# Kernel optimization log

Measured on AMD Instinct MI355X. Metric: run time of the kernel, lower is better.

## Reference

```python
import jax, jax.numpy as jnp
import numpy as np

N_NODES = 100000
N_EDGES = 3200000
IN_FEAT = 256   # dim * decoder_heads = 128 * 2
HEADS = 2
N_CLASSES = 8
CURV = 1.0
NEG_SLOPE = 0.2
EPS = 1e-15


def setup_inputs() -> dict:
    key = jax.random.key(0)
    ks = jax.random.split(key, 7)
    x = jax.random.normal(ks[0], (N_NODES, IN_FEAT), dtype=jnp.float32) * 0.1
    edge_index = jax.random.randint(ks[1], (2, N_EDGES), 0, N_NODES, dtype=jnp.int64)
    W = jax.random.normal(ks[2], (IN_FEAT, HEADS * N_CLASSES), dtype=jnp.float32) * (1.0 / np.sqrt(IN_FEAT))
    attn_l = jax.random.normal(ks[3], (HEADS, N_CLASSES), dtype=jnp.float32) * 0.1
    attn_r = jax.random.normal(ks[4], (HEADS, N_CLASSES), dtype=jnp.float32) * 0.1
    bias = jnp.zeros((HEADS, N_CLASSES), dtype=jnp.float32)
    W_res = jax.random.normal(ks[5], (IN_FEAT, HEADS * N_CLASSES), dtype=jnp.float32) * (1.0 / np.sqrt(IN_FEAT))
    return {"x": x, "edge_index": edge_index, "W": W, "attn_l": attn_l,
            "attn_r": attn_r, "bias": bias, "W_res": W_res}


def _artanh(z):
    z = jnp.clip(z, -1.0 + 1e-7, 1.0 - 1e-7)
    return 0.5 * (jnp.log1p(z) - jnp.log1p(-z))


def _logmap0_poincare(x, c):
    # PoincareBall.logmap0; proj_tan0 is identity for the Poincare ball.
    sqrt_c = jnp.sqrt(c)
    norm = jnp.maximum(jnp.linalg.norm(x, axis=-1, keepdims=True), EPS)
    scale = _artanh(sqrt_c * norm) / (sqrt_c * norm)
    return scale * x


def reference(x, edge_index, W, attn_l, attn_r, bias, W_res):
    N = x.shape[0]
    # hyperbolic -> tangent space at origin
    h = _logmap0_poincare(x, CURV)                               # [N, F]
    # GATConv (DGL-style), dropout disabled (eval)
    feat = (h @ W).reshape(N, HEADS, N_CLASSES)                  # [N, H, C]
    el = jnp.einsum('nhc,hc->nh', feat, attn_l)                  # [N, H]
    er = jnp.einsum('nhc,hc->nh', feat, attn_r)                  # [N, H]
    src, dst = edge_index[0], edge_index[1]
    e = el[src] + er[dst]                                        # [E, H]
    e = jnp.where(e >= 0, e, NEG_SLOPE * e)                      # leaky_relu
    # edge softmax over incoming edges of each destination node
    m = jax.ops.segment_max(e, dst, num_segments=N)              # [N, H]
    m = jnp.where(jnp.isfinite(m), m, 0.0)
    e_exp = jnp.exp(e - m[dst])                                  # [E, H]
    denom = jax.ops.segment_sum(e_exp, dst, num_segments=N)      # [N, H]
    alpha = e_exp / jnp.maximum(denom[dst], EPS)                 # [E, H]
    # aggregate messages
    msg = alpha[:, :, None] * feat[src]                          # [E, H, C]
    rst = jax.ops.segment_sum(msg, dst, num_segments=N)          # [N, H, C]
    # residual + bias
    rst = rst + (h @ W_res).reshape(N, HEADS, N_CLASSES) + bias
    # Decoder.decode: probs.mean(dim=1) over heads
    return rst.mean(axis=1)                                      # [N, C]
```

## Files before the change

### kernel.cpp

```cpp
#include <hip/hip_runtime.h>
#include <math.h>

#define N_NODES 100000
#define N_EDGES 3200000
#define IN_FEAT 256
#define HEADS 2
#define NC 8
#define FH 16
#define NEG_SLOPE 0.2f
#define EPSF 1e-15f

#define BSH 7
#define BUCK_W 128
#define DLM 127
#define NBUCK ((N_NODES + BUCK_W - 1) / BUCK_W)
#define B1 200
#define EPB (N_EDGES / B1)

#define SORT_CAP 5120
#define RCAP (SORT_CAP / 256)

typedef float f32x4 __attribute__((ext_vector_type(4)));
typedef short bf16x8 __attribute__((ext_vector_type(8)));

__device__ __forceinline__ unsigned short f2bf(float f) {
    unsigned u = __float_as_uint(f);
    u += 0x7FFFu + ((u >> 16) & 1u);
    return (unsigned short)(u >> 16);
}
__device__ __forceinline__ float bflo(unsigned u) { return __uint_as_float(u << 16); }
__device__ __forceinline__ float bfhi(unsigned u) { return __uint_as_float(u & 0xFFFF0000u); }

__global__ __launch_bounds__(256) void k_node(
        const float* __restrict__ x, const float* __restrict__ W,
        const float* __restrict__ Wres, const float* __restrict__ attn_l,
        const float* __restrict__ attn_r,
        unsigned short* __restrict__ featb, float* __restrict__ res,
        float* __restrict__ el, float* __restrict__ er) {
    int wid = (blockIdx.x * 256 + threadIdx.x) >> 6;
    int n0 = wid * 16;
    if (n0 >= N_NODES) return;
    int l   = threadIdx.x & 63;
    int col = l & 15;
    int g   = l >> 4;

    bf16x8 bw[8], bq[8];
    #pragma unroll
    for (int kk = 0; kk < 8; kk++) {
        #pragma unroll
        for (int j = 0; j < 8; j++) {
            int k = kk * 32 + g * 8 + j;
            bw[kk][j] = (short)f2bf(W[k * FH + col]);
            bq[kk][j] = (short)f2bf(Wres[k * FH + col]);
        }
    }

    const float* xr = x + (size_t)(n0 + col) * IN_FEAT;
    f32x4 acc0 = {0.f, 0.f, 0.f, 0.f};
    f32x4 acc1 = {0.f, 0.f, 0.f, 0.f};
    float ss = 0.f;
    #pragma unroll
    for (int kk = 0; kk < 8; kk++) {
        float4 v0 = *(const float4*)(xr + kk * 32 + g * 8);
        float4 v1 = *(const float4*)(xr + kk * 32 + g * 8 + 4);
        ss += v0.x * v0.x + v0.y * v0.y + v0.z * v0.z + v0.w * v0.w
            + v1.x * v1.x + v1.y * v1.y + v1.z * v1.z + v1.w * v1.w;
        bf16x8 a;
        a[0] = (short)f2bf(v0.x); a[1] = (short)f2bf(v0.y);
        a[2] = (short)f2bf(v0.z); a[3] = (short)f2bf(v0.w);
        a[4] = (short)f2bf(v1.x); a[5] = (short)f2bf(v1.y);
        a[6] = (short)f2bf(v1.z); a[7] = (short)f2bf(v1.w);
        acc0 = __builtin_amdgcn_mfma_f32_16x16x32_bf16(a, bw[kk], acc0, 0, 0, 0);
        acc1 = __builtin_amdgcn_mfma_f32_16x16x32_bf16(a, bq[kk], acc1, 0, 0, 0);
    }

    ss += __shfl_xor(ss, 16);
    ss += __shfl_xor(ss, 32);
    float norm = fmaxf(sqrtf(ss), EPSF);
    float z = fminf(norm, 1.f - 1e-7f);
    float at = 0.5f * (log1pf(z) - log1pf(-z));
    float scale = at / norm;

    float alc = attn_l[col], arc = attn_r[col];

    #pragma unroll
    for (int i = 0; i < 4; i++) {
        int ri = g * 4 + i;
        float s_i = __shfl(scale, ri);
        int nr = n0 + ri;
        float f_i = acc0[i] * s_i;
        float q_i = acc1[i] * s_i;
        featb[(size_t)nr * FH + col] = f2bf(f_i);
        res  [(size_t)nr * FH + col] = q_i;
        float pl = f_i * alc, pr = f_i * arc;
        float pl0 = (col < 8) ? pl : 0.f, pl1 = (col < 8) ? 0.f : pl;
        float pr0 = (col < 8) ? pr : 0.f, pr1 = (col < 8) ? 0.f : pr;
        #pragma unroll
        for (int m = 1; m < 16; m <<= 1) {
            pl0 += __shfl_xor(pl0, m); pl1 += __shfl_xor(pl1, m);
            pr0 += __shfl_xor(pr0, m); pr1 += __shfl_xor(pr1, m);
        }
        if (col == 0) {
            *(float2*)(el + nr * 2) = make_float2(pl0, pl1);
            *(float2*)(er + nr * 2) = make_float2(pr0, pr1);
        }
    }
}

__global__ __launch_bounds__(256) void k_count(const int* __restrict__ ei,
                                               int* __restrict__ hist_g) {
    __shared__ int h[NBUCK];
    for (int i = threadIdx.x; i < NBUCK; i += 256) h[i] = 0;
    __syncthreads();
    const int4* dp = (const int4*)(ei + N_EDGES + (size_t)blockIdx.x * EPB);
    for (int i = threadIdx.x; i < EPB / 4; i += 256) {
        int4 d = dp[i];
        atomicAdd(&h[d.x >> BSH], 1);
        atomicAdd(&h[d.y >> BSH], 1);
        atomicAdd(&h[d.z >> BSH], 1);
        atomicAdd(&h[d.w >> BSH], 1);
    }
    __syncthreads();
    int* outp = hist_g + (size_t)blockIdx.x * NBUCK;
    for (int i = threadIdx.x; i < NBUCK; i += 256) outp[i] = h[i];
}

__global__ __launch_bounds__(64) void k_scan1(int* __restrict__ hist_g,
                                              int* __restrict__ btot) {
    __shared__ int sm[64];
    int bucket = blockIdx.x;
    int t = threadIdx.x;
    int carry = 0;
    for (int base = 0; base < B1; base += 64) {
        int blk = base + t;
        int v = (blk < B1) ? hist_g[(size_t)blk * NBUCK + bucket] : 0;
        __syncthreads();
        sm[t] = v;
        __syncthreads();
        for (int off = 1; off < 64; off <<= 1) {
            int u = (t >= off) ? sm[t - off] : 0;
            __syncthreads();
            sm[t] += u;
            __syncthreads();
        }
        if (blk < B1) hist_g[(size_t)blk * NBUCK + bucket] = carry + sm[t] - v;
        carry += sm[63];
    }
    if (t == 0) btot[bucket] = carry;
}

__global__ __launch_bounds__(1024) void k_scan2(const int* __restrict__ btot,
                                                int* __restrict__ bstart) {
    __shared__ int sm[1024];
    int t = threadIdx.x;
    int v = (t < NBUCK) ? btot[t] : 0;
    sm[t] = v;
    __syncthreads();
    for (int off = 1; off < 1024; off <<= 1) {
        int u = (t >= off) ? sm[t - off] : 0;
        __syncthreads();
        sm[t] += u;
        __syncthreads();
    }
    if (t < NBUCK) bstart[t] = sm[t] - v;
    if (t == 1023) bstart[NBUCK] = sm[1023];
}

__global__ __launch_bounds__(256) void k_scatter2(const int* __restrict__ ei,
                                                  const int* __restrict__ hist_g,
                                                  const int* __restrict__ bstart,
                                                  unsigned* __restrict__ packed) {
    __shared__ int cur[NBUCK];
    const int* hrow = hist_g + (size_t)blockIdx.x * NBUCK;
    for (int i = threadIdx.x; i < NBUCK; i += 256) cur[i] = bstart[i] + hrow[i];
    __syncthreads();
    size_t e0 = (size_t)blockIdx.x * EPB;
    const int4* sp = (const int4*)(ei + e0);
    const int4* dp = (const int4*)(ei + N_EDGES + e0);
    for (int i = threadIdx.x; i < EPB / 4; i += 256) {
        int4 s = sp[i];
        int4 d = dp[i];
        int p0 = atomicAdd(&cur[d.x >> BSH], 1);
        int p1 = atomicAdd(&cur[d.y >> BSH], 1);
        int p2 = atomicAdd(&cur[d.z >> BSH], 1);
        int p3 = atomicAdd(&cur[d.w >> BSH], 1);
        packed[p0] = (unsigned)s.x | ((unsigned)(d.x & DLM) << 17);
        packed[p1] = (unsigned)s.y | ((unsigned)(d.y & DLM) << 17);
        packed[p2] = (unsigned)s.z | ((unsigned)(d.z & DLM) << 17);
        packed[p3] = (unsigned)s.w | ((unsigned)(d.w & DLM) << 17);
    }
}

__global__ __launch_bounds__(256) void k_aggsort(
        const unsigned* __restrict__ packed, const int* __restrict__ bstart,
        const float* __restrict__ el, const float* __restrict__ er,
        const unsigned short* __restrict__ featb, const float* __restrict__ res,
        const float* __restrict__ bias, float* __restrict__ out) {
    __shared__ int cnt[BUCK_W];
    __shared__ int off[BUCK_W];
    __shared__ unsigned srt[SORT_CAP];
    int b = blockIdx.x, t = threadIdx.x;
    int lo = bstart[b], hi = bstart[b + 1];

    if (t < BUCK_W) cnt[t] = 0;
    __syncthreads();

    unsigned pe[RCAP];
    int      tk[RCAP];
    #pragma unroll
    for (int i = 0; i < RCAP; i++) {
        int j = lo + i * 256 + t;
        if (j < hi) {
            unsigned p = packed[j];
            pe[i] = p;
            tk[i] = atomicAdd(&cnt[p >> 17], 1);
        } else {
            pe[i] = 0u; tk[i] = -1;
        }
    }
    __syncthreads();

    if (t < BUCK_W) off[t] = cnt[t];
    __syncthreads();
    #pragma unroll
    for (int d = 1; d < BUCK_W; d <<= 1) {
        int v = (t < BUCK_W && t >= d) ? off[t - d] : 0;
        __syncthreads();
        if (t < BUCK_W) off[t] += v;
        __syncthreads();
    }

    #pragma unroll
    for (int i = 0; i < RCAP; i++) {
        if (tk[i] >= 0) {
            int dl = (int)(pe[i] >> 17);
            srt[off[dl] - cnt[dl] + tk[i]] = pe[i] & 0x1FFFFu;
        }
    }
    __syncthreads();

    int dl = t >> 1, r = t & 1;
    int n = b * BUCK_W + dl;
    if (n >= N_NODES) return;
    int sBeg = off[dl] - cnt[dl];
    int sEnd = off[dl];
    float2 ern = *(const float2*)(er + n * 2);
    float den0 = 0.f, den1 = 0.f;
    float S[FH];
    #pragma unroll
    for (int k = 0; k < FH; k++) S[k] = 0.f;

    int j = sBeg + r;
    for (; j + 2 < sEnd; j += 4) {
        int sa = (int)srt[j], sb = (int)srt[j + 2];
        float2 ea = *(const float2*)(el + sa * 2);
        float2 eb = *(const float2*)(el + sb * 2);
        const uint4* fpa = (const uint4*)(featb + (size_t)sa * FH);
        const uint4* fpb = (const uint4*)(featb + (size_t)sb * FH);
        uint4 ua0 = fpa[0], ua1 = fpa[1];
        uint4 ub0 = fpb[0], ub1 = fpb[1];
        float va0 = ea.x + ern.x, va1 = ea.y + ern.y;
        float vb0 = eb.x + ern.x, vb1 = eb.y + ern.y;
        va0 = va0 >= 0.f ? va0 : NEG_SLOPE * va0;
        va1 = va1 >= 0.f ? va1 : NEG_SLOPE * va1;
        vb0 = vb0 >= 0.f ? vb0 : NEG_SLOPE * vb0;
        vb1 = vb1 >= 0.f ? vb1 : NEG_SLOPE * vb1;
        float wa0 = __expf(va0), wa1 = __expf(va1);
        float wb0 = __expf(vb0), wb1 = __expf(vb1);
        den0 += wa0 + wb0; den1 += wa1 + wb1;
        S[0]  = fmaf(wa0, bflo(ua0.x), fmaf(wb0, bflo(ub0.x), S[0]));
        S[1]  = fmaf(wa0, bfhi(ua0.x), fmaf(wb0, bfhi(ub0.x), S[1]));
        S[2]  = fmaf(wa0, bflo(ua0.y), fmaf(wb0, bflo(ub0.y), S[2]));
        S[3]  = fmaf(wa0, bfhi(ua0.y), fmaf(wb0, bfhi(ub0.y), S[3]));
        S[4]  = fmaf(wa0, bflo(ua0.z), fmaf(wb0, bflo(ub0.z), S[4]));
        S[5]  = fmaf(wa0, bfhi(ua0.z), fmaf(wb0, bfhi(ub0.z), S[5]));
        S[6]  = fmaf(wa0, bflo(ua0.w), fmaf(wb0, bflo(ub0.w), S[6]));
        S[7]  = fmaf(wa0, bfhi(ua0.w), fmaf(wb0, bfhi(ub0.w), S[7]));
        S[8]  = fmaf(wa1, bflo(ua1.x), fmaf(wb1, bflo(ub1.x), S[8]));
        S[9]  = fmaf(wa1, bfhi(ua1.x), fmaf(wb1, bfhi(ub1.x), S[9]));
        S[10] = fmaf(wa1, bflo(ua1.y), fmaf(wb1, bflo(ub1.y), S[10]));
        S[11] = fmaf(wa1, bfhi(ua1.y), fmaf(wb1, bfhi(ub1.y), S[11]));
        S[12] = fmaf(wa1, bflo(ua1.z), fmaf(wb1, bflo(ub1.z), S[12]));
        S[13] = fmaf(wa1, bfhi(ua1.z), fmaf(wb1, bfhi(ub1.z), S[13]));
        S[14] = fmaf(wa1, bflo(ua1.w), fmaf(wb1, bflo(ub1.w), S[14]));
        S[15] = fmaf(wa1, bfhi(ua1.w), fmaf(wb1, bfhi(ub1.w), S[15]));
    }
    for (; j < sEnd; j += 2) {
        int sa = (int)srt[j];
        float2 ea = *(const float2*)(el + sa * 2);
        float v0 = ea.x + ern.x, v1 = ea.y + ern.y;
        v0 = v0 >= 0.f ? v0 : NEG_SLOPE * v0;
        v1 = v1 >= 0.f ? v1 : NEG_SLOPE * v1;
        float w0 = __expf(v0), w1 = __expf(v1);
        den0 += w0; den1 += w1;
        const uint4* fp = (const uint4*)(featb + (size_t)sa * FH);
        uint4 u0 = fp[0], u1 = fp[1];
        S[0]  = fmaf(w0, bflo(u0.x), S[0]);  S[1]  = fmaf(w0, bfhi(u0.x), S[1]);
        S[2]  = fmaf(w0, bflo(u0.y), S[2]);  S[3]  = fmaf(w0, bfhi(u0.y), S[3]);
        S[4]  = fmaf(w0, bflo(u0.z), S[4]);  S[5]  = fmaf(w0, bfhi(u0.z), S[5]);
        S[6]  = fmaf(w0, bflo(u0.w), S[6]);  S[7]  = fmaf(w0, bfhi(u0.w), S[7]);
        S[8]  = fmaf(w1, bflo(u1.x), S[8]);  S[9]  = fmaf(w1, bfhi(u1.x), S[9]);
        S[10] = fmaf(w1, bflo(u1.y), S[10]); S[11] = fmaf(w1, bfhi(u1.y), S[11]);
        S[12] = fmaf(w1, bflo(u1.z), S[12]); S[13] = fmaf(w1, bfhi(u1.z), S[13]);
        S[14] = fmaf(w1, bflo(u1.w), S[14]); S[15] = fmaf(w1, bfhi(u1.w), S[15]);
    }

    #pragma unroll
    for (int k = 0; k < FH; k++) S[k] += __shfl_xor(S[k], 1);
    den0 += __shfl_xor(den0, 1);
    den1 += __shfl_xor(den1, 1);

    if (r == 0) {
        float inv0 = 1.f / fmaxf(den0, EPSF);
        float inv1 = 1.f / fmaxf(den1, EPSF);
        const float* rr = res + (size_t)n * FH;
        float4 r0a = *(const float4*)(rr + 0),  r0b = *(const float4*)(rr + 4);
        float4 r1a = *(const float4*)(rr + 8),  r1b = *(const float4*)(rr + 12);
        float4 oa, ob;
        oa.x = 0.5f * ((S[0] * inv0 + r0a.x + bias[0])  + (S[8]  * inv1 + r1a.x + bias[8]));
        oa.y = 0.5f * ((S[1] * inv0 + r0a.y + bias[1])  + (S[9]  * inv1 + r1a.y + bias[9]));
        oa.z = 0.5f * ((S[2] * inv0 + r0a.z + bias[2])  + (S[10] * inv1 + r1a.z + bias[10]));
        oa.w = 0.5f * ((S[3] * inv0 + r0a.w + bias[3])  + (S[11] * inv1 + r1a.w + bias[11]));
        ob.x = 0.5f * ((S[4] * inv0 + r0b.x + bias[4])  + (S[12] * inv1 + r1b.x + bias[12]));
        ob.y = 0.5f * ((S[5] * inv0 + r0b.y + bias[5])  + (S[13] * inv1 + r1b.y + bias[13]));
        ob.z = 0.5f * ((S[6] * inv0 + r0b.z + bias[6])  + (S[14] * inv1 + r1b.z + bias[14]));
        ob.w = 0.5f * ((S[7] * inv0 + r0b.w + bias[7])  + (S[15] * inv1 + r1b.w + bias[15]));
        *(float4*)(out + (size_t)n * NC + 0) = oa;
        *(float4*)(out + (size_t)n * NC + 4) = ob;
    }
}

extern "C" void kernel_launch(void* const* d_in, const int* in_sizes, int n_in,
                              void* d_out, int out_size, void* d_ws, size_t ws_size,
                              hipStream_t stream) {
    const float* x      = (const float*)d_in[0];
    const int*   ei     = (const int*)d_in[1];
    const float* W      = (const float*)d_in[2];
    const float* attn_l = (const float*)d_in[3];
    const float* attn_r = (const float*)d_in[4];
    const float* bias   = (const float*)d_in[5];
    const float* Wres   = (const float*)d_in[6];
    float* out = (float*)d_out;

    char* ws = (char*)d_ws;
    const size_t szFB   = (size_t)N_NODES * FH * sizeof(unsigned short);
    const size_t szNF   = (size_t)N_NODES * FH * sizeof(float);
    const size_t szNH   = (size_t)N_NODES * HEADS * sizeof(float);
    const size_t szHist = ((size_t)B1 * NBUCK * sizeof(int) + 255) & ~(size_t)255;
    const size_t szBt   = 4096;
    size_t off = 0;
    unsigned short* featb = (unsigned short*)(ws + off); off += szFB;
    float*    res    = (float*)(ws + off); off += szNF;
    float*    el     = (float*)(ws + off); off += szNH;
    float*    er     = (float*)(ws + off); off += szNH;
    int*      hist_g = (int*)  (ws + off); off += szHist;
    int*      btot   = (int*)  (ws + off); off += szBt;
    int*      bstart = (int*)  (ws + off); off += szBt;
    unsigned* packed = (unsigned*)(ws + off); off += (size_t)N_EDGES * sizeof(unsigned);

    k_node<<<(N_NODES / 16 + 3) / 4, 256, 0, stream>>>(x, W, Wres, attn_l, attn_r,
                                                       featb, res, el, er);
    k_count<<<B1, 256, 0, stream>>>(ei, hist_g);
    k_scan1<<<NBUCK, 64, 0, stream>>>(hist_g, btot);
    k_scan2<<<1, 1024, 0, stream>>>(btot, bstart);
    k_scatter2<<<B1, 256, 0, stream>>>(ei, hist_g, bstart, packed);
    k_aggsort<<<NBUCK, 256, 0, stream>>>(packed, bstart, el, er, featb, res, bias, out);
}
```

Measured before the change: 122.0 us.

## Fuse count/scan/scatter partition into one cooperative kernel with grid syncs

Replaces the four partition kernels (count, two scans, scatter) with a single cooperative kernel of 500 blocks that keeps each block's edges in registers, builds its histogram, grid-syncs, scans per bucket, grid-syncs, has every block redundantly scan bucket totals, then scatters from registers. This removes three launches and the second read of the edge index. It relies on cooperative launch with 500 resident blocks and adds grid-wide barrier cost. Chunks are remapped by XCD to spread work across dies.

```diff
diff --git a/kernel.cpp b/kernel.cpp
--- a/kernel.cpp
+++ b/kernel.cpp
@@ -1,4 +1,5 @@
 #include <hip/hip_runtime.h>
+#include <hip/hip_cooperative_groups.h>
 #include <math.h>
 
 #define N_NODES 100000
@@ -14,8 +15,10 @@
 #define BUCK_W 128
 #define DLM 127
 #define NBUCK ((N_NODES + BUCK_W - 1) / BUCK_W)
-#define B1 200
-#define EPB (N_EDGES / B1)
+
+#define B1F 500
+#define EPBF (N_EDGES / B1F)
+#define RC (EPBF / 256)
 
 #define SORT_CAP 5120
 #define RCAP (SORT_CAP / 256)
@@ -107,88 +110,92 @@
     }
 }
 
-__global__ __launch_bounds__(256) void k_count(const int* __restrict__ ei,
-                                               int* __restrict__ hist_g) {
-    __shared__ int h[NBUCK];
-    for (int i = threadIdx.x; i < NBUCK; i += 256) h[i] = 0;
-    __syncthreads();
-    const int4* dp = (const int4*)(ei + N_EDGES + (size_t)blockIdx.x * EPB);
-    for (int i = threadIdx.x; i < EPB / 4; i += 256) {
-        int4 d = dp[i];
-        atomicAdd(&h[d.x >> BSH], 1);
-        atomicAdd(&h[d.y >> BSH], 1);
-        atomicAdd(&h[d.z >> BSH], 1);
-        atomicAdd(&h[d.w >> BSH], 1);
-    }
-    __syncthreads();
-    int* outp = hist_g + (size_t)blockIdx.x * NBUCK;
-    for (int i = threadIdx.x; i < NBUCK; i += 256) outp[i] = h[i];
-}
-
-__global__ __launch_bounds__(64) void k_scan1(int* __restrict__ hist_g,
-                                              int* __restrict__ btot) {
-    __shared__ int sm[64];
-    int bucket = blockIdx.x;
+__global__ __launch_bounds__(256, 2) void k_part(
+        const int* __restrict__ ei, int* __restrict__ hist_g,
+        int* __restrict__ btot, int* __restrict__ bstart_g,
+        unsigned* __restrict__ packed) {
+    cooperative_groups::grid_group grid = cooperative_groups::this_grid();
+    __shared__ int cnt[NBUCK];
+    __shared__ int sb[1024];
     int t = threadIdx.x;
-    int carry = 0;
-    for (int base = 0; base < B1; base += 64) {
-        int blk = base + t;
-        int v = (blk < B1) ? hist_g[(size_t)blk * NBUCK + bucket] : 0;
-        __syncthreads();
-        sm[t] = v;
-        __syncthreads();
-        for (int off = 1; off < 64; off <<= 1) {
-            int u = (t >= off) ? sm[t - off] : 0;
+    int bid = blockIdx.x;
+    int xcd = bid & 7, q = bid >> 3;
+    int chunk = (xcd < 4) ? (xcd * 63 + q) : (252 + (xcd - 4) * 62 + q);
+
+    for (int k = t; k < NBUCK; k += 256) cnt[k] = 0;
+    __syncthreads();
+    unsigned pw[RC]; int bk[RC], tk[RC];
+    int e0 = chunk * EPBF;
+    #pragma unroll
+    for (int i = 0; i < RC; i++) {
+        int j = e0 + i * 256 + t;
+        int s = ei[j];
+        int d = ei[N_EDGES + j];
+        bk[i] = d >> BSH;
+        pw[i] = (unsigned)s | ((unsigned)(d & DLM) << 17);
+        tk[i] = atomicAdd(&cnt[bk[i]], 1);
+    }
+    __syncthreads();
+    int* hrow = hist_g + (size_t)chunk * NBUCK;
+    for (int k = t; k < NBUCK; k += 256) hrow[k] = cnt[k];
+
+    grid.sync();
+
+    for (int c = bid; c < NBUCK; c += B1F) {
+        int t2 = t + 256;
+        int v0 = hist_g[(size_t)t * NBUCK + c];
+        int v1 = (t2 < B1F) ? hist_g[(size_t)t2 * NBUCK + c] : 0;
+        sb[t] = v0; sb[t2] = v1;
+        __syncthreads();
+        for (int d = 1; d < 512; d <<= 1) {
+            int a0 = (t  >= d) ? sb[t  - d] : 0;
+            int a1 = (t2 >= d) ? sb[t2 - d] : 0;
             __syncthreads();
-            sm[t] += u;
+            sb[t] += a0; sb[t2] += a1;
             __syncthreads();
         }
-        if (blk < B1) hist_g[(size_t)blk * NBUCK + bucket] = carry + sm[t] - v;
-        carry += sm[63];
-    }
-    if (t == 0) btot[bucket] = carry;
-}
-
-__global__ __launch_bounds__(1024) void k_scan2(const int* __restrict__ btot,
-                                                int* __restrict__ bstart) {
-    __shared__ int sm[1024];
-    int t = threadIdx.x;
-    int v = (t < NBUCK) ? btot[t] : 0;
-    sm[t] = v;
-    __syncthreads();
-    for (int off = 1; off < 1024; off <<= 1) {
-        int u = (t >= off) ? sm[t - off] : 0;
-        __syncthreads();
-        sm[t] += u;
-        __syncthreads();
-    }
-    if (t < NBUCK) bstart[t] = sm[t] - v;
-    if (t == 1023) bstart[NBUCK] = sm[1023];
-}
-
-__global__ __launch_bounds__(256) void k_scatter2(const int* __restrict__ ei,
-                                                  const int* __restrict__ hist_g,
-                                                  const int* __restrict__ bstart,
-                                                  unsigned* __restrict__ packed) {
-    __shared__ int cur[NBUCK];
-    const int* hrow = hist_g + (size_t)blockIdx.x * NBUCK;
-    for (int i = threadIdx.x; i < NBUCK; i += 256) cur[i] = bstart[i] + hrow[i];
-    __syncthreads();
-    size_t e0 = (size_t)blockIdx.x * EPB;
-    const int4* sp = (const int4*)(ei + e0);
-    const int4* dp = (const int4*)(ei + N_EDGES + e0);
-    for (int i = threadIdx.x; i < EPB / 4; i += 256) {
-        int4 s = sp[i];
-        int4 d = dp[i];
-        int p0 = atomicAdd(&cur[d.x >> BSH], 1);
-        int p1 = atomicAdd(&cur[d.y >> BSH], 1);
-        int p2 = atomicAdd(&cur[d.z >> BSH], 1);
-        int p3 = atomicAdd(&cur[d.w >> BSH], 1);
-        packed[p0] = (unsigned)s.x | ((unsigned)(d.x & DLM) << 17);
-        packed[p1] = (unsigned)s.y | ((unsigned)(d.y & DLM) << 17);
-        packed[p2] = (unsigned)s.z | ((unsigned)(d.z & DLM) << 17);
-        packed[p3] = (unsigned)s.w | ((unsigned)(d.w & DLM) << 17);
-    }
+        hist_g[(size_t)t * NBUCK + c] = sb[t] - v0;
+        if (t2 < B1F) hist_g[(size_t)t2 * NBUCK + c] = sb[t2] - v1;
+        if (t == 0) btot[c] = sb[511];
+        __syncthreads();
+    }
+
+    grid.sync();
+
+    int o[4];
+    #pragma unroll
+    for (int j = 0; j < 4; j++) {
+        int idx = t + j * 256;
+        o[j] = (idx < NBUCK) ? btot[idx] : 0;
+        sb[idx] = o[j];
+    }
+    __syncthreads();
+    for (int d = 1; d < 1024; d <<= 1) {
+        int a[4];
+        #pragma unroll
+        for (int j = 0; j < 4; j++) {
+            int idx = t + j * 256;
+            a[j] = (idx >= d) ? sb[idx - d] : 0;
+        }
+        __syncthreads();
+        #pragma unroll
+        for (int j = 0; j < 4; j++) sb[t + j * 256] += a[j];
+        __syncthreads();
+    }
+    #pragma unroll
+    for (int j = 0; j < 4; j++) {
+        int idx = t + j * 256;
+        if (idx < NBUCK) {
+            int bst = sb[idx] - o[j];
+            cnt[idx] = bst + hrow[idx];
+            if (bid == 0) bstart_g[idx] = bst;
+        }
+    }
+    if (bid == 0 && t == 0) bstart_g[NBUCK] = N_EDGES;
+    __syncthreads();
+    #pragma unroll
+    for (int i = 0; i < RC; i++)
+        packed[cnt[bk[i]] + tk[i]] = pw[i];
 }
 
 __global__ __launch_bounds__(256) void k_aggsort(
@@ -252,11 +259,11 @@
 
     int j = sBeg + r;
     for (; j + 2 < sEnd; j += 4) {
-        int sa = (int)srt[j], sb = (int)srt[j + 2];
+        int sa = (int)srt[j], sb2 = (int)srt[j + 2];
         float2 ea = *(const float2*)(el + sa * 2);
-        float2 eb = *(const float2*)(el + sb * 2);
+        float2 eb = *(const float2*)(el + sb2 * 2);
         const uint4* fpa = (const uint4*)(featb + (size_t)sa * FH);
-        const uint4* fpb = (const uint4*)(featb + (size_t)sb * FH);
+        const uint4* fpb = (const uint4*)(featb + (size_t)sb2 * FH);
         uint4 ua0 = fpa[0], ua1 = fpa[1];
         uint4 ub0 = fpb[0], ub1 = fpb[1];
         float va0 = ea.x + ern.x, va1 = ea.y + ern.y;
@@ -346,7 +353,7 @@
     const size_t szFB   = (size_t)N_NODES * FH * sizeof(unsigned short);
     const size_t szNF   = (size_t)N_NODES * FH * sizeof(float);
     const size_t szNH   = (size_t)N_NODES * HEADS * sizeof(float);
-    const size_t szHist = ((size_t)B1 * NBUCK * sizeof(int) + 255) & ~(size_t)255;
+    const size_t szHist = (((size_t)B1F * NBUCK * sizeof(int)) + 255) & ~(size_t)255;
     const size_t szBt   = 4096;
     size_t off = 0;
     unsigned short* featb = (unsigned short*)(ws + off); off += szFB;
@@ -360,9 +367,11 @@
 
     k_node<<<(N_NODES / 16 + 3) / 4, 256, 0, stream>>>(x, W, Wres, attn_l, attn_r,
                                                        featb, res, el, er);
-    k_count<<<B1, 256, 0, stream>>>(ei, hist_g);
-    k_scan1<<<NBUCK, 64, 0, stream>>>(hist_g, btot);
-    k_scan2<<<1, 1024, 0, stream>>>(btot, bstart);
-    k_scatter2<<<B1, 256, 0, stream>>>(ei, hist_g, bstart, packed);
+    {
+        void* args[] = {(void*)&ei, (void*)&hist_g, (void*)&btot,
+                        (void*)&bstart, (void*)&packed};
+        hipLaunchCooperativeKernel((void*)k_part, dim3(B1F), dim3(256),
+                                   args, 0, stream);
+    }
     k_aggsort<<<NBUCK, 256, 0, stream>>>(packed, bstart, el, er, featb, res, bias, out);
 }
```

Measured after the change: 239.2 us. 96.0% more time.
